# Kernel tuning notes

Measured on AMD Instinct MI355X. Metric: run time of the kernel, lower is better.

The kernel has to match this reference:

```python
import jax, jax.numpy as jnp
import numpy as np

N, E, C, NA, NR, H = 50000, 320000, 64, 10, 8, 64
AVG_NUM_NEIGHBORS = 16.0
WEIGHT_NUMEL = 5 * C  # 5 uvu tensor-product paths, one weight per channel


def setup_inputs() -> dict:
    key = jax.random.key(0)
    ks = jax.random.split(key, 18)
    rn = lambda k, s: jax.random.normal(k, s, dtype=jnp.float32)
    return {
        "node_attrs": jax.random.uniform(ks[0], (N, NA), dtype=jnp.float32),
        "node_feats_s": rn(ks[1], (N, C)),
        "node_feats_v": rn(ks[2], (N, C, 3)),
        "edge_sh0": jnp.ones((E, 1), jnp.float32),          # Y_00 (constant)
        "edge_sh1": rn(ks[3], (E, 3)),                       # Y_1m
        "edge_feats": rn(ks[4], (E, NR)),                    # radial scalars (0e)
        "senders": jax.random.randint(ks[5], (E,), 0, N, dtype=jnp.int32),
        "receivers": jax.random.randint(ks[6], (E,), 0, N, dtype=jnp.int32),
        # skip-connection tensor-product linear: (C*NA)x0e -> Cx0e, (C*NA)x1o -> Cx1o
        "W_sc_s": rn(ks[7], (C * NA, C)),
        "W_sc_v": rn(ks[8], (C * NA, C)),
        # self linear on node_feats (per-irrep channel mixing)
        "W_self_s": rn(ks[9], (C, C)),
        "W_self_v": rn(ks[10], (C, C)),
        # radial MLP: NR -> 64 -> 64 -> 64 -> weight_numel
        "W1": rn(ks[11], (NR, H)),
        "W2": rn(ks[12], (H, H)),
        "W3": rn(ks[13], (H, H)),
        "W4": rn(ks[14], (H, WEIGHT_NUMEL)),
        # output linear: mid irreps 2Cx0e + 3Cx1o -> target Cx0e + Cx1o
        "W_out_s": rn(ks[15], (2 * C, C)),
        "W_out_v": rn(ks[16], (3 * C, C)),
    }


def reference(node_attrs, node_feats_s, node_feats_v, edge_sh0, edge_sh1,
              edge_feats, senders, receivers, W_sc_s, W_sc_v, W_self_s,
              W_self_v, W1, W2, W3, W4, W_out_s, W_out_v):
    n, c = node_feats_s.shape
    na = node_attrs.shape[1]
    # ---- skip connection: Linear(hidden)(node_feats (x) node_attrs) ----
    ts = (node_feats_s[:, :, None] * node_attrs[:, None, :]).reshape(n, c * na)
    tv = (node_feats_v[:, :, None, :] * node_attrs[:, None, :, None]).reshape(n, c * na, 3)
    inv_sc = 1.0 / np.sqrt(c * na)
    sc_s = (ts @ W_sc_s) * inv_sc
    sc_v = jnp.einsum('nkx,kd->ndx', tv, W_sc_v) * inv_sc
    # ---- self linear on node_feats ----
    inv_c = 1.0 / np.sqrt(c)
    s = (node_feats_s @ W_self_s) * inv_c
    v = jnp.einsum('ncx,cd->ndx', node_feats_v, W_self_v) * inv_c
    # ---- radial MLP -> per-edge tensor-product weights ----
    h = jax.nn.silu((edge_feats @ W1) / np.sqrt(edge_feats.shape[1]))
    h = jax.nn.silu((h @ W2) / np.sqrt(H))
    h = jax.nn.silu((h @ W3) / np.sqrt(H))
    w = (h @ W4) / np.sqrt(H)                      # [E, 5C]
    w1, w2, w3, w4, w5 = jnp.split(w, 5, axis=1)   # one weight per path per channel
    # ---- gather -> per-edge equivariant tensor product -> scatter-add ----
    se = s[senders]                                # [E, C]
    ve = v[senders]                                # [E, C, 3]
    p1 = w1 * se * edge_sh0                                              # 0e x 0e -> 0e
    p2 = w2 * jnp.einsum('ecx,ex->ec', ve, edge_sh1) / np.sqrt(3.0)      # 1o x 1o -> 0e
    p3 = (w3 * se)[:, :, None] * edge_sh1[:, None, :]                    # 0e x 1o -> 1o
    p4 = (w4 * edge_sh0)[:, :, None] * ve                                # 1o x 0e -> 1o
    p5 = w5[:, :, None] * jnp.cross(ve, edge_sh1[:, None, :]) / np.sqrt(2.0)  # 1o x 1o -> 1o
    mji_s = jnp.concatenate([p1, p2], axis=1)      # [E, 2C]
    mji_v = jnp.concatenate([p3, p4, p5], axis=1)  # [E, 3C, 3]
    m_s = jnp.zeros((n, 2 * c), mji_s.dtype).at[receivers].add(mji_s)
    m_v = jnp.zeros((n, 3 * c, 3), mji_v.dtype).at[receivers].add(mji_v)
    # ---- output linear / avg_num_neighbors ----
    out_s = (m_s @ W_out_s) / (np.sqrt(2 * c) * AVG_NUM_NEIGHBORS)
    out_v = jnp.einsum('nkx,kd->ndx', m_v, W_out_v) / (np.sqrt(3 * c) * AVG_NUM_NEIGHBORS)
    return (out_s, out_v, sc_s, sc_v)
```

## Files before the change

### kernel.cpp

```cpp
#include <hip/hip_runtime.h>

#define NC    64
#define NATTR 10
#define NH    64
#define NRAD  8
#define TEB   128
#define MPN   704

__device__ __forceinline__ float silu_f(float x) { return x / (1.0f + __expf(-x)); }

typedef __fp16 h2v __attribute__((ext_vector_type(2)));

__device__ __forceinline__ unsigned int pkh(float lo, float hi)
{
    union { h2v h; unsigned int u; } cv;
    cv.h = __builtin_amdgcn_cvt_pkrtz(lo, hi);
    return cv.u;
}
__device__ __forceinline__ h2v uph(unsigned int u)
{
    union { unsigned int u; h2v h; } cv;
    cv.u = u;
    return cv.h;
}

#if defined(__has_builtin)
#if __has_builtin(__builtin_amdgcn_fdot2)
#define HAS_FDOT2 1
#endif
#endif

__device__ __forceinline__ float fd2(unsigned int a, unsigned int b, float c)
{
#ifdef HAS_FDOT2
    return __builtin_amdgcn_fdot2(uph(a), uph(b), c, false);
#else
    h2v x = uph(a), y = uph(b);
    return c + (float)x[0] * (float)y[0] + (float)x[1] * (float)y[1];
#endif
}

__device__ __forceinline__ void dot2w(const uint4* hp,
    const unsigned int (&Wa)[32], const unsigned int (&Wb)[32],
    float& ra, float& rb)
{
    float a = 0.f, b = 0.f;
    #pragma unroll
    for (int q8 = 0; q8 < 8; q8++) {
        uint4 hu = hp[q8];
        unsigned int hw[4] = {hu.x, hu.y, hu.z, hu.w};
        #pragma unroll
        for (int k = 0; k < 4; k++) {
            a = fd2(hw[k], Wa[q8 * 4 + k], a);
            b = fd2(hw[k], Wb[q8 * 4 + k], b);
        }
    }
    ra = a * 0.125f; rb = b * 0.125f;
}

__device__ __forceinline__ void dot3w(const uint4* hp,
    const unsigned int (&Wa)[32], const unsigned int (&Wb)[32],
    const unsigned int (&Wc)[32],
    float& ra, float& rb, float& rc)
{
    float a = 0.f, b = 0.f, c = 0.f;
    #pragma unroll
    for (int q8 = 0; q8 < 8; q8++) {
        uint4 hu = hp[q8];
        unsigned int hw[4] = {hu.x, hu.y, hu.z, hu.w};
        #pragma unroll
        for (int k = 0; k < 4; k++) {
            a = fd2(hw[k], Wa[q8 * 4 + k], a);
            b = fd2(hw[k], Wb[q8 * 4 + k], b);
            c = fd2(hw[k], Wc[q8 * 4 + k], c);
        }
    }
    ra = a * 0.125f; rb = b * 0.125f; rc = c * 0.125f;
}


__global__ void hist_kernel(const int* __restrict__ rcv, int* __restrict__ deg, int E)
{
    int e = blockIdx.x * 256 + threadIdx.x;
    if (e < E) atomicAdd(&deg[rcv[e]], 1);
}

__global__ __launch_bounds__(256)
void scan_kernel(const int* __restrict__ deg, int* __restrict__ row_ptr, int N)
{
    __shared__ int sums[256];
    __shared__ int offs[257];
    const int t = threadIdx.x;
    const int chunk = (N + 255) / 256;
    int b = t * chunk, e = min(N, b + chunk);
    int s = 0;
    for (int k = b; k < e; k++) s += deg[k];
    sums[t] = s;
    __syncthreads();
    if (t == 0) {
        int run = 0;
        for (int i = 0; i < 256; i++) { offs[i] = run; run += sums[i]; }
        offs[256] = run;
    }
    __syncthreads();
    int run = offs[t];
    for (int k = b; k < e; k++) { row_ptr[k] = run; run += deg[k]; }
    if (t == 255) row_ptr[N] = offs[256];
}

__global__ void fill_kernel(const int* __restrict__ rcv, const int* __restrict__ row_ptr,
                            int* __restrict__ cursor, int* __restrict__ eidx, int E)
{
    int e = blockIdx.x * 256 + threadIdx.x;
    if (e < E) {
        int r = rcv[e];
        int pos = atomicAdd(&cursor[r], 1);
        eidx[row_ptr[r] + pos] = e;
    }
}

__global__ __launch_bounds__(256)
void self_kernel(const float* __restrict__ fs, const float* __restrict__ fv,
                 const float* __restrict__ Wes, const float* __restrict__ Wev,
                 float* __restrict__ out, int N)
{
    __shared__ float s_l[4][NC];
    __shared__ float v_l[4][3][NC];
    const int t = threadIdx.x, wv = t >> 6, lane = t & 63;
    const int n = blockIdx.x * 4 + wv;

    if (n < N) {
        s_l[wv][lane] = fs[(size_t)n * NC + lane];
        v_l[wv][0][lane] = fv[(size_t)n * NC * 3 + lane * 3 + 0];
        v_l[wv][1][lane] = fv[(size_t)n * NC * 3 + lane * 3 + 1];
        v_l[wv][2][lane] = fv[(size_t)n * NC * 3 + lane * 3 + 2];
    }
    __syncthreads();
    if (n >= N) return;

    const int d = lane;
    float a = 0.f, bx = 0.f, by = 0.f, bz = 0.f;
    #pragma unroll 8
    for (int c = 0; c < NC; c++) {
        float ws = Wes[c * NC + d];
        float wvv = Wev[c * NC + d];
        a  += s_l[wv][c] * ws;
        bx += v_l[wv][0][c] * wvv;
        by += v_l[wv][1][c] * wvv;
        bz += v_l[wv][2][c] * wvv;
    }
    out[(size_t)N * 256 + (size_t)n * NC + d]            = a  * 0.125f;
    out[(size_t)N * 320 + (size_t)n * 192 +       d]     = bx * 0.125f;
    out[(size_t)N * 320 + (size_t)n * 192 +  64 + d]     = by * 0.125f;
    out[(size_t)N * 320 + (size_t)n * 192 + 128 + d]     = bz * 0.125f;
}

__global__ __launch_bounds__(128, 3)
void edge_kernel(const float* __restrict__ ef, const float* __restrict__ sh0,
                 const float* __restrict__ sh1,
                 const int* __restrict__ snd, const int* __restrict__ rcv,
                 const float* __restrict__ W1, const float* __restrict__ W2,
                 const float* __restrict__ W3, const float* __restrict__ W4,
                 const float* __restrict__ s_st, const float* __restrict__ v_st,
                 const int* __restrict__ eidx,
                 float* __restrict__ m, int E)
{
    __shared__ unsigned int h_l[TEB][36];
    __shared__ float sh1_l[TEB][3];
    __shared__ float sh0_l[TEB];
    __shared__ int   snd_l[TEB];
    __shared__ int   rcv_l[TEB];

    const int t = threadIdx.x;
    const int p0 = blockIdx.x * TEB;

    {
        int p = p0 + t;
        bool valid = p < E;
        int e = valid ? eidx[p] : 0;
        snd_l[t] = valid ? snd[e] : 0;
        rcv_l[t] = valid ? rcv[e] : -1;
        sh0_l[t] = valid ? sh0[e] : 0.f;
        sh1_l[t][0] = valid ? sh1[(size_t)e * 3 + 0] : 0.f;
        sh1_l[t][1] = valid ? sh1[(size_t)e * 3 + 1] : 0.f;
        sh1_l[t][2] = valid ? sh1[(size_t)e * 3 + 2] : 0.f;

        float x[NRAD];
        #pragma unroll
        for (int r = 0; r < NRAD; r++)
            x[r] = valid ? ef[(size_t)e * NRAD + r] : 0.f;

        float h1[NH];
        #pragma unroll
        for (int j = 0; j < NH; j++) {
            float a = 0.f;
            #pragma unroll
            for (int r = 0; r < NRAD; r++) a += x[r] * W1[r * NH + j];
            h1[j] = silu_f(a * 0.35355339059327373f);
        }

        unsigned int h2p[32];
        for (int jt = 0; jt < 16; jt++) {
            float a0 = 0.f, a1 = 0.f, a2 = 0.f, a3 = 0.f;
            #pragma unroll
            for (int c = 0; c < NH; c++) {
                float hv = h1[c];
                const float* wr = W2 + c * NH + jt * 4;
                a0 += hv * wr[0]; a1 += hv * wr[1];
                a2 += hv * wr[2]; a3 += hv * wr[3];
            }
            h2p[jt * 2 + 0] = pkh(silu_f(a0 * 0.125f), silu_f(a1 * 0.125f));
            h2p[jt * 2 + 1] = pkh(silu_f(a2 * 0.125f), silu_f(a3 * 0.125f));
        }
        for (int jt = 0; jt < 16; jt++) {
            float a0 = 0.f, a1 = 0.f, a2 = 0.f, a3 = 0.f;
            #pragma unroll
            for (int cp = 0; cp < 32; cp++) {
                h2v u = uph(h2p[cp]);
                float hl = (float)u[0], hh = (float)u[1];
                const float* wr0 = W3 + (2 * cp) * NH + jt * 4;
                const float* wr1 = W3 + (2 * cp + 1) * NH + jt * 4;
                a0 += hl * wr0[0] + hh * wr1[0];
                a1 += hl * wr0[1] + hh * wr1[1];
                a2 += hl * wr0[2] + hh * wr1[2];
                a3 += hl * wr0[3] + hh * wr1[3];
            }
            h_l[t][jt * 2 + 0] = pkh(silu_f(a0 * 0.125f), silu_f(a1 * 0.125f));
            h_l[t][jt * 2 + 1] = pkh(silu_f(a2 * 0.125f), silu_f(a3 * 0.125f));
        }
    }
    __syncthreads();

    const int wv = t >> 6, lane = t & 63;
    const int base = wv * 64;
    const int v_sd = snd_l[base + lane];
    const int v_rc = rcv_l[base + lane];

    {
        unsigned int WA[32], WC[32];
        #pragma unroll
        for (int q = 0; q < 32; q++) {
            WA[q] = pkh(W4[(2 * q) * 320 + lane],       W4[(2 * q + 1) * 320 + lane]);
            WC[q] = pkh(W4[(2 * q) * 320 + 128 + lane], W4[(2 * q + 1) * 320 + 128 + lane]);
        }
        #pragma unroll
        for (int q = 0; q < 32; q++) {
            asm volatile("" : "+v"(WA[q]));
            asm volatile("" : "+v"(WC[q]));
        }
        float g0 = s_st[(size_t)__builtin_amdgcn_readlane(v_sd, 0) * NC + lane];
        float g1 = s_st[(size_t)__builtin_amdgcn_readlane(v_sd, 1) * NC + lane];
        float g2 = s_st[(size_t)__builtin_amdgcn_readlane(v_sd, 2) * NC + lane];
        float g3 = s_st[(size_t)__builtin_amdgcn_readlane(v_sd, 3) * NC + lane];
        int r_cur = -1;
        float a1 = 0.f, a3x = 0.f, a3y = 0.f, a3z = 0.f;
        #pragma unroll 4
        for (int ei = 0; ei < 64; ei++) {
            const int pn = (ei + 4 > 63) ? 63 : ei + 4;
            const float gf = s_st[(size_t)__builtin_amdgcn_readlane(v_sd, pn) * NC + lane];
            const int r = __builtin_amdgcn_readlane(v_rc, ei);
            if (r != r_cur) {
                if (r_cur >= 0) {
                    float* mb = m + (size_t)r_cur * MPN;
                    unsafeAtomicAdd(mb + lane,             a1);
                    unsafeAtomicAdd(mb + 128 + lane,       a3x);
                    unsafeAtomicAdd(mb + 128 + 192 + lane, a3y);
                    unsafeAtomicAdd(mb + 128 + 384 + lane, a3z);
                    a1 = a3x = a3y = a3z = 0.f;
                }
                r_cur = r;
            }
            if (r >= 0) {
                const int pos = base + ei;
                float w1w, w3w;
                dot2w((const uint4*)(&h_l[pos][0]), WA, WC, w1w, w3w);
                float se = g0;
                a1 += w1w * se * sh0_l[pos];
                float t3 = w3w * se;
                a3x += t3 * sh1_l[pos][0];
                a3y += t3 * sh1_l[pos][1];
                a3z += t3 * sh1_l[pos][2];
            }
            g0 = g1; g1 = g2; g2 = g3; g3 = gf;
        }
        if (r_cur >= 0) {
            float* mb = m + (size_t)r_cur * MPN;
            unsafeAtomicAdd(mb + lane,             a1);
            unsafeAtomicAdd(mb + 128 + lane,       a3x);
            unsafeAtomicAdd(mb + 128 + 192 + lane, a3y);
            unsafeAtomicAdd(mb + 128 + 384 + lane, a3z);
        }
    }

    {
        unsigned int WB[32], WD[32], WE[32];
        #pragma unroll
        for (int q = 0; q < 32; q++) {
            WB[q] = pkh(W4[(2 * q) * 320 +  64 + lane], W4[(2 * q + 1) * 320 +  64 + lane]);
            WD[q] = pkh(W4[(2 * q) * 320 + 192 + lane], W4[(2 * q + 1) * 320 + 192 + lane]);
            WE[q] = pkh(W4[(2 * q) * 320 + 256 + lane], W4[(2 * q + 1) * 320 + 256 + lane]);
        }
        #pragma unroll
        for (int q = 0; q < 32; q++) {
            asm volatile("" : "+v"(WB[q]));
            asm volatile("" : "+v"(WD[q]));
            asm volatile("" : "+v"(WE[q]));
        }
        float gx0, gy0, gz0, gx1, gy1, gz1, gx2, gy2, gz2, gx3, gy3, gz3;
        {
            size_t s0 = (size_t)__builtin_amdgcn_readlane(v_sd, 0) * 192;
            size_t s1 = (size_t)__builtin_amdgcn_readlane(v_sd, 1) * 192;
            size_t s2 = (size_t)__builtin_amdgcn_readlane(v_sd, 2) * 192;
            size_t s3 = (size_t)__builtin_amdgcn_readlane(v_sd, 3) * 192;
            gx0 = v_st[s0 + lane]; gy0 = v_st[s0 + 64 + lane]; gz0 = v_st[s0 + 128 + lane];
            gx1 = v_st[s1 + lane]; gy1 = v_st[s1 + 64 + lane]; gz1 = v_st[s1 + 128 + lane];
            gx2 = v_st[s2 + lane]; gy2 = v_st[s2 + 64 + lane]; gz2 = v_st[s2 + 128 + lane];
            gx3 = v_st[s3 + lane]; gy3 = v_st[s3 + 64 + lane]; gz3 = v_st[s3 + 128 + lane];
        }
        int r_cur = -1;
        float a2 = 0.f;
        float a4x = 0.f, a4y = 0.f, a4z = 0.f;
        float a5x = 0.f, a5y = 0.f, a5z = 0.f;
        #pragma unroll 4
        for (int ei = 0; ei < 64; ei++) {
            const int pn = (ei + 4 > 63) ? 63 : ei + 4;
            size_t sb = (size_t)__builtin_amdgcn_readlane(v_sd, pn) * 192;
            const float gxf = v_st[sb + lane];
            const float gyf = v_st[sb + 64 + lane];
            const float gzf = v_st[sb + 128 + lane];
            const int r = __builtin_amdgcn_readlane(v_rc, ei);
            if (r != r_cur) {
                if (r_cur >= 0) {
                    float* mb = m + (size_t)r_cur * MPN;
                    unsafeAtomicAdd(mb + 64 + lane,              a2);
                    unsafeAtomicAdd(mb + 128 + 64 + lane,        a4x);
                    unsafeAtomicAdd(mb + 128 + 192 + 64 + lane,  a4y);
                    unsafeAtomicAdd(mb + 128 + 384 + 64 + lane,  a4z);
                    unsafeAtomicAdd(mb + 128 + 128 + lane,       a5x);
                    unsafeAtomicAdd(mb + 128 + 192 + 128 + lane, a5y);
                    unsafeAtomicAdd(mb + 128 + 384 + 128 + lane, a5z);
                    a2 = a4x = a4y = a4z = a5x = a5y = a5z = 0.f;
                }
                r_cur = r;
            }
            if (r >= 0) {
                const int pos = base + ei;
                float w2w, w4w, w5w;
                dot3w((const uint4*)(&h_l[pos][0]), WB, WD, WE, w2w, w4w, w5w);
                float vx = gx0, vy = gy0, vz = gz0;
                float shx = sh1_l[pos][0], shy = sh1_l[pos][1], shz = sh1_l[pos][2];
                float dot = vx * shx + vy * shy + vz * shz;
                a2 += w2w * dot * 0.5773502691896258f;
                float w4s = w4w * sh0_l[pos];
                a4x += w4s * vx; a4y += w4s * vy; a4z += w4s * vz;
                float w5s = w5w * 0.7071067811865476f;
                a5x += w5s * (vy * shz - vz * shy);
                a5y += w5s * (vz * shx - vx * shz);
                a5z += w5s * (vx * shy - vy * shx);
            }
            gx0 = gx1; gy0 = gy1; gz0 = gz1;
            gx1 = gx2; gy1 = gy2; gz1 = gz2;
            gx2 = gx3; gy2 = gy3; gz2 = gz3;
            gx3 = gxf; gy3 = gyf; gz3 = gzf;
        }
        if (r_cur >= 0) {
            float* mb = m + (size_t)r_cur * MPN;
            unsafeAtomicAdd(mb + 64 + lane,              a2);
            unsafeAtomicAdd(mb + 128 + 64 + lane,        a4x);
            unsafeAtomicAdd(mb + 128 + 192 + 64 + lane,  a4y);
            unsafeAtomicAdd(mb + 128 + 384 + 64 + lane,  a4z);
            unsafeAtomicAdd(mb + 128 + 128 + lane,       a5x);
            unsafeAtomicAdd(mb + 128 + 192 + 128 + lane, a5y);
            unsafeAtomicAdd(mb + 128 + 384 + 128 + lane, a5z);
        }
    }
}

__global__ __launch_bounds__(256)
void sc_kernel(const float* __restrict__ attrs, const float* __restrict__ fs,
               const float* __restrict__ fv,
               const float* __restrict__ Wss, const float* __restrict__ Wsv,
               float* __restrict__ out, int N)
{
    __shared__ unsigned int At[32][68];
    __shared__ unsigned int Bt[32][68];

    const int part = blockIdx.y;
    const int n0 = blockIdx.x * 64;
    const int t = threadIdx.x;
    const int tn = t & 15, td = t >> 4;
    const float* W = (part == 0) ? Wss : Wsv;
    const int x = part - 1;

    float acc[4][4];
    #pragma unroll
    for (int i = 0; i < 4; i++)
        #pragma unroll
        for (int j = 0; j < 4; j++) acc[i][j] = 0.f;

    for (int kt = 0; kt < 10; kt++) {
        __syncthreads();
        for (int i = t; i < 2048; i += 256) {
            int n = i >> 5, kp = i & 31;
            int k0 = kt * 64 + kp * 2;
            int c0 = k0 / 10, a0 = k0 - c0 * 10;
            int k1 = k0 + 1;
            int c1 = k1 / 10, a1 = k1 - c1 * 10;
            int ng = n0 + n;
            float f0 = 0.f, f1 = 0.f;
            if (ng < N) {
                float fa = (part == 0) ? fs[(size_t)ng * 64 + c0]
                                       : fv[((size_t)ng * 64 + c0) * 3 + x];
                float fb = (part == 0) ? fs[(size_t)ng * 64 + c1]
                                       : fv[((size_t)ng * 64 + c1) * 3 + x];
                f0 = fa * attrs[(size_t)ng * 10 + a0];
                f1 = fb * attrs[(size_t)ng * 10 + a1];
            }
            At[kp][n] = pkh(f0, f1);
        }
        for (int i = t; i < 2048; i += 256) {
            int kp = i >> 6, d = i & 63;
            Bt[kp][d] = pkh(W[(size_t)(kt * 64 + 2 * kp) * 64 + d],
                            W[(size_t)(kt * 64 + 2 * kp + 1) * 64 + d]);
        }
        __syncthreads();
        #pragma unroll 8
        for (int kp = 0; kp < 32; kp++) {
            uint4 au = *(const uint4*)(&At[kp][tn * 4]);
            uint4 bu = *(const uint4*)(&Bt[kp][td * 4]);
            unsigned int aa[4] = {au.x, au.y, au.z, au.w};
            unsigned int bb[4] = {bu.x, bu.y, bu.z, bu.w};
            #pragma unroll
            for (int i = 0; i < 4; i++)
                #pragma unroll
                for (int j = 0; j < 4; j++)
                    acc[i][j] = fd2(aa[i], bb[j], acc[i][j]);
        }
    }

    const float inv_sc = 0.03952847075210474f;
    #pragma unroll
    for (int i = 0; i < 4; i++) {
        int ng = n0 + tn * 4 + i;
        if (ng >= N) continue;
        #pragma unroll
        for (int j = 0; j < 4; j++) {
            int d = td * 4 + j;
            float v = acc[i][j] * inv_sc;
            if (part == 0) out[(size_t)N * 256 + (size_t)ng * 64 + d] = v;
            else           out[(size_t)N * 320 + (size_t)ng * 192 + d * 3 + x] = v;
        }
    }
}

__global__ __launch_bounds__(256)
void outlin_kernel(const float* __restrict__ m,
                   const float* __restrict__ Wos, const float* __restrict__ Wov,
                   float* __restrict__ out, int N)
{
    __shared__ unsigned int At[32][68];
    __shared__ unsigned int Bt[32][68];

    const int part = blockIdx.y;
    const int n0 = blockIdx.x * 64;
    const int t = threadIdx.x;
    const int tn = t & 15, td = t >> 4;
    const int x = part - 1;
    const int ntiles = (part == 0) ? 2 : 3;
    const int aoff = (part == 0) ? 0 : 128 + x * 192;
    const float* W = (part == 0) ? Wos : Wov;

    float acc[4][4];
    #pragma unroll
    for (int i = 0; i < 4; i++)
        #pragma unroll
        for (int j = 0; j < 4; j++) acc[i][j] = 0.f;

    for (int kt = 0; kt < ntiles; kt++) {
        __syncthreads();
        for (int i = t; i < 2048; i += 256) {
            int n = i >> 5, kp = i & 31;
            int ng = n0 + n;
            float f0 = 0.f, f1 = 0.f;
            if (ng < N) {
                const float* mp = m + (size_t)ng * MPN + aoff + kt * 64 + kp * 2;
                f0 = mp[0]; f1 = mp[1];
            }
            At[kp][n] = pkh(f0, f1);
        }
        for (int i = t; i < 2048; i += 256) {
            int kp = i >> 6, d = i & 63;
            Bt[kp][d] = pkh(W[(size_t)(kt * 64 + 2 * kp) * 64 + d],
                            W[(size_t)(kt * 64 + 2 * kp + 1) * 64 + d]);
        }
        __syncthreads();
        #pragma unroll 8
        for (int kp = 0; kp < 32; kp++) {
            uint4 au = *(const uint4*)(&At[kp][tn * 4]);
            uint4 bu = *(const uint4*)(&Bt[kp][td * 4]);
            unsigned int aa[4] = {au.x, au.y, au.z, au.w};
            unsigned int bb[4] = {bu.x, bu.y, bu.z, bu.w};
            #pragma unroll
            for (int i = 0; i < 4; i++)
                #pragma unroll
                for (int j = 0; j < 4; j++)
                    acc[i][j] = fd2(aa[i], bb[j], acc[i][j]);
        }
    }

    const float scale = (part == 0) ? 0.005524271728019903f
                                    : 0.004510527174164819f;
    #pragma unroll
    for (int i = 0; i < 4; i++) {
        int ng = n0 + tn * 4 + i;
        if (ng >= N) continue;
        #pragma unroll
        for (int j = 0; j < 4; j++) {
            int d = td * 4 + j;
            float v = acc[i][j] * scale;
            if (part == 0) out[(size_t)ng * 64 + d] = v;
            else           out[(size_t)N * 64 + (size_t)ng * 192 + d * 3 + x] = v;
        }
    }
}

extern "C" void kernel_launch(void* const* d_in, const int* in_sizes, int n_in,
                              void* d_out, int out_size, void* d_ws, size_t ws_size,
                              hipStream_t stream)
{
    const float* attrs = (const float*)d_in[0];
    const float* fs    = (const float*)d_in[1];
    const float* fv    = (const float*)d_in[2];
    const float* sh0   = (const float*)d_in[3];
    const float* sh1   = (const float*)d_in[4];
    const float* ef    = (const float*)d_in[5];
    const int*   snd   = (const int*)d_in[6];
    const int*   rcv   = (const int*)d_in[7];
    const float* Wss   = (const float*)d_in[8];
    const float* Wsv   = (const float*)d_in[9];
    const float* Wes   = (const float*)d_in[10];
    const float* Wev   = (const float*)d_in[11];
    const float* W1    = (const float*)d_in[12];
    const float* W2    = (const float*)d_in[13];
    const float* W3    = (const float*)d_in[14];
    const float* W4    = (const float*)d_in[15];
    const float* Wos   = (const float*)d_in[16];
    const float* Wov   = (const float*)d_in[17];

    const int N = in_sizes[0] / NATTR;
    const int E = in_sizes[6];

    float* out = (float*)d_out;
    const float* s_st = out + (size_t)N * 256;
    const float* v_st = out + (size_t)N * 320;

    int* deg     = (int*)d_out;
    int* cursor  = deg + N;
    int* row_ptr = cursor + N;
    int* eidx    = row_ptr + N + 1;

    float* m = (float*)d_ws;

    (void)hipMemsetAsync(deg, 0, (size_t)2 * N * sizeof(int), stream);
    (void)hipMemsetAsync(m, 0, (size_t)N * MPN * sizeof(float), stream);

    const int eb = (E + 255) / 256;
    hist_kernel<<<eb, 256, 0, stream>>>(rcv, deg, E);
    scan_kernel<<<1, 256, 0, stream>>>(deg, row_ptr, N);
    fill_kernel<<<eb, 256, 0, stream>>>(rcv, row_ptr, cursor, eidx, E);

    self_kernel<<<(N + 3) / 4, 256, 0, stream>>>(fs, fv, Wes, Wev, out, N);

    const int nbe = (E + TEB - 1) / TEB;
    edge_kernel<<<nbe, 128, 0, stream>>>(ef, sh0, sh1, snd, rcv,
                                         W1, W2, W3, W4, s_st, v_st,
                                         eidx, m, E);

    dim3 g_out((N + 63) / 64, 4);
    outlin_kernel<<<g_out, 256, 0, stream>>>(m, Wos, Wov, out, N);

    dim3 g_sc((N + 63) / 64, 4);
    sc_kernel<<<g_sc, 256, 0, stream>>>(attrs, fs, fv, Wss, Wsv, out, N);
}
```

Before: 1.073 ms.

## Merge skip-connection and output-linear GEMMs into one kernel with larger node tiles

Replaces the separate sc_kernel and outlin_kernel with one post_kernel. It launches on a grid of 8 parts and uses 256-node tiles with a 16x4 register accumulator per thread, so each loaded weight tile is reused across four times as many nodes. The edge kernel also packs sh0 and sh1 into one float4 shared array so a single vector LDS load replaces four scalar loads. Costs are higher register pressure and more LDS per block, which lowers occupancy, plus fewer and larger blocks that can cause load imbalance between the sc and outlin parts.

```diff
diff --git a/kernel.cpp b/kernel.cpp
--- a/kernel.cpp
+++ b/kernel.cpp
@@ -166,8 +166,7 @@
                  float* __restrict__ m, int E)
 {
     __shared__ unsigned int h_l[TEB][36];
-    __shared__ float sh1_l[TEB][3];
-    __shared__ float sh0_l[TEB];
+    __shared__ float sh_l[TEB][4];
     __shared__ int   snd_l[TEB];
     __shared__ int   rcv_l[TEB];
 
@@ -180,10 +179,10 @@
         int e = valid ? eidx[p] : 0;
         snd_l[t] = valid ? snd[e] : 0;
         rcv_l[t] = valid ? rcv[e] : -1;
-        sh0_l[t] = valid ? sh0[e] : 0.f;
-        sh1_l[t][0] = valid ? sh1[(size_t)e * 3 + 0] : 0.f;
-        sh1_l[t][1] = valid ? sh1[(size_t)e * 3 + 1] : 0.f;
-        sh1_l[t][2] = valid ? sh1[(size_t)e * 3 + 2] : 0.f;
+        sh_l[t][0] = valid ? sh0[e] : 0.f;
+        sh_l[t][1] = valid ? sh1[(size_t)e * 3 + 0] : 0.f;
+        sh_l[t][2] = valid ? sh1[(size_t)e * 3 + 1] : 0.f;
+        sh_l[t][3] = valid ? sh1[(size_t)e * 3 + 2] : 0.f;
 
         float x[NRAD];
         #pragma unroll
@@ -274,12 +273,13 @@
                 const int pos = base + ei;
                 float w1w, w3w;
                 dot2w((const uint4*)(&h_l[pos][0]), WA, WC, w1w, w3w);
+                float4 sh4 = *(const float4*)(&sh_l[pos][0]);
                 float se = g0;
-                a1 += w1w * se * sh0_l[pos];
+                a1 += w1w * se * sh4.x;
                 float t3 = w3w * se;
-                a3x += t3 * sh1_l[pos][0];
-                a3y += t3 * sh1_l[pos][1];
-                a3z += t3 * sh1_l[pos][2];
+                a3x += t3 * sh4.y;
+                a3y += t3 * sh4.z;
+                a3z += t3 * sh4.w;
             }
             g0 = g1; g1 = g2; g2 = g3; g3 = gf;
         }
@@ -347,16 +347,16 @@
                 const int pos = base + ei;
                 float w2w, w4w, w5w;
                 dot3w((const uint4*)(&h_l[pos][0]), WB, WD, WE, w2w, w4w, w5w);
+                float4 sh4 = *(const float4*)(&sh_l[pos][0]);
                 float vx = gx0, vy = gy0, vz = gz0;
-                float shx = sh1_l[pos][0], shy = sh1_l[pos][1], shz = sh1_l[pos][2];
-                float dot = vx * shx + vy * shy + vz * shz;
+                float dot = vx * sh4.y + vy * sh4.z + vz * sh4.w;
                 a2 += w2w * dot * 0.5773502691896258f;
-                float w4s = w4w * sh0_l[pos];
+                float w4s = w4w * sh4.x;
                 a4x += w4s * vx; a4y += w4s * vy; a4z += w4s * vz;
                 float w5s = w5w * 0.7071067811865476f;
-                a5x += w5s * (vy * shz - vz * shy);
-                a5y += w5s * (vz * shx - vx * shz);
-                a5z += w5s * (vx * shy - vy * shx);
+                a5x += w5s * (vy * sh4.w - vz * sh4.z);
+                a5y += w5s * (vz * sh4.y - vx * sh4.w);
+                a5z += w5s * (vx * sh4.z - vy * sh4.y);
             }
             gx0 = gx1; gy0 = gy1; gz0 = gz1;
             gx1 = gx2; gy1 = gy2; gz1 = gz2;
@@ -377,46 +377,71 @@
 }
 
 __global__ __launch_bounds__(256)
-void sc_kernel(const float* __restrict__ attrs, const float* __restrict__ fs,
-               const float* __restrict__ fv,
-               const float* __restrict__ Wss, const float* __restrict__ Wsv,
-               float* __restrict__ out, int N)
-{
-    __shared__ unsigned int At[32][68];
+void post_kernel(const float* __restrict__ attrs, const float* __restrict__ fs,
+                 const float* __restrict__ fv,
+                 const float* __restrict__ Wss, const float* __restrict__ Wsv,
+                 const float* __restrict__ m,
+                 const float* __restrict__ Wos, const float* __restrict__ Wov,
+                 float* __restrict__ out, int N)
+{
+    __shared__ unsigned int At[32][260];
     __shared__ unsigned int Bt[32][68];
 
-    const int part = blockIdx.y;
-    const int n0 = blockIdx.x * 64;
+    const int y = blockIdx.y;
+    const bool is_sc = (y < 4);
+    const int part = is_sc ? y : y - 4;
+    const int n0 = blockIdx.x * 256;
     const int t = threadIdx.x;
     const int tn = t & 15, td = t >> 4;
-    const float* W = (part == 0) ? Wss : Wsv;
     const int x = part - 1;
 
-    float acc[4][4];
+    const float* W;
+    int nkt, aoff = 0;
+    if (is_sc) { W = (part == 0) ? Wss : Wsv; nkt = 10; }
+    else {
+        W = (part == 0) ? Wos : Wov;
+        nkt = (part == 0) ? 2 : 3;
+        aoff = (part == 0) ? 0 : 128 + x * 192;
+    }
+
+    float acc[16][4];
     #pragma unroll
-    for (int i = 0; i < 4; i++)
+    for (int i = 0; i < 16; i++)
         #pragma unroll
         for (int j = 0; j < 4; j++) acc[i][j] = 0.f;
 
-    for (int kt = 0; kt < 10; kt++) {
+    for (int kt = 0; kt < nkt; kt++) {
         __syncthreads();
-        for (int i = t; i < 2048; i += 256) {
-            int n = i >> 5, kp = i & 31;
-            int k0 = kt * 64 + kp * 2;
-            int c0 = k0 / 10, a0 = k0 - c0 * 10;
-            int k1 = k0 + 1;
-            int c1 = k1 / 10, a1 = k1 - c1 * 10;
-            int ng = n0 + n;
-            float f0 = 0.f, f1 = 0.f;
-            if (ng < N) {
-                float fa = (part == 0) ? fs[(size_t)ng * 64 + c0]
-                                       : fv[((size_t)ng * 64 + c0) * 3 + x];
-                float fb = (part == 0) ? fs[(size_t)ng * 64 + c1]
-                                       : fv[((size_t)ng * 64 + c1) * 3 + x];
-                f0 = fa * attrs[(size_t)ng * 10 + a0];
-                f1 = fb * attrs[(size_t)ng * 10 + a1];
-            }
-            At[kp][n] = pkh(f0, f1);
+        if (is_sc) {
+            for (int i = t; i < 8192; i += 256) {
+                int n = i >> 5, kp = i & 31;
+                int k0 = kt * 64 + kp * 2;
+                int c0 = k0 / 10, am0 = k0 - c0 * 10;
+                int k1 = k0 + 1;
+                int c1 = k1 / 10, am1 = k1 - c1 * 10;
+                int ng = n0 + n;
+                float f0 = 0.f, f1 = 0.f;
+                if (ng < N) {
+                    float fa = (part == 0) ? fs[(size_t)ng * 64 + c0]
+                                           : fv[((size_t)ng * 64 + c0) * 3 + x];
+                    float fb = (part == 0) ? fs[(size_t)ng * 64 + c1]
+                                           : fv[((size_t)ng * 64 + c1) * 3 + x];
+                    f0 = fa * attrs[(size_t)ng * 10 + am0];
+                    f1 = fb * attrs[(size_t)ng * 10 + am1];
+                }
+                At[kp][n] = pkh(f0, f1);
+            }
+        } else {
+            for (int i = t; i < 8192; i += 256) {
+                int n = i >> 5, kp = i & 31;
+                int ng = n0 + n;
+                float f0 = 0.f, f1 = 0.f;
+                if (ng < N) {
+                    const float* mp = m + (size_t)ng * MPN + aoff + kt * 64 + kp * 2;
+                    f0 = mp[0]; f1 = mp[1];
+                }
+                At[kp][n] = pkh(f0, f1);
+            }
         }
         for (int i = t; i < 2048; i += 256) {
             int kp = i >> 6, d = i & 63;
@@ -424,102 +449,46 @@
                             W[(size_t)(kt * 64 + 2 * kp + 1) * 64 + d]);
         }
         __syncthreads();
-        #pragma unroll 8
+        #pragma unroll 4
         for (int kp = 0; kp < 32; kp++) {
-            uint4 au = *(const uint4*)(&At[kp][tn * 4]);
             uint4 bu = *(const uint4*)(&Bt[kp][td * 4]);
-            unsigned int aa[4] = {au.x, au.y, au.z, au.w};
             unsigned int bb[4] = {bu.x, bu.y, bu.z, bu.w};
             #pragma unroll
-            for (int i = 0; i < 4; i++)
+            for (int sb = 0; sb < 4; sb++) {
+                uint4 au = *(const uint4*)(&At[kp][sb * 64 + tn * 4]);
+                unsigned int aa[4] = {au.x, au.y, au.z, au.w};
                 #pragma unroll
-                for (int j = 0; j < 4; j++)
-                    acc[i][j] = fd2(aa[i], bb[j], acc[i][j]);
-        }
-    }
-
-    const float inv_sc = 0.03952847075210474f;
+                for (int i = 0; i < 4; i++)
+                    #pragma unroll
+                    for (int j = 0; j < 4; j++)
+                        acc[sb * 4 + i][j] = fd2(aa[i], bb[j], acc[sb * 4 + i][j]);
+            }
+        }
+    }
+
+    float scale;
+    if (is_sc) scale = 0.03952847075210474f;
+    else scale = (part == 0) ? 0.005524271728019903f
+                             : 0.004510527174164819f;
+
     #pragma unroll
-    for (int i = 0; i < 4; i++) {
-        int ng = n0 + tn * 4 + i;
-        if (ng >= N) continue;
-        #pragma unroll
-        for (int j = 0; j < 4; j++) {
-            int d = td * 4 + j;
-            float v = acc[i][j] * inv_sc;
-            if (part == 0) out[(size_t)N * 256 + (size_t)ng * 64 + d] = v;
-            else           out[(size_t)N * 320 + (size_t)ng * 192 + d * 3 + x] = v;
-        }
-    }
-}
-
-__global__ __launch_bounds__(256)
-void outlin_kernel(const float* __restrict__ m,
-                   const float* __restrict__ Wos, const float* __restrict__ Wov,
-                   float* __restrict__ out, int N)
-{
-    __shared__ unsigned int At[32][68];
-    __shared__ unsigned int Bt[32][68];
-
-    const int part = blockIdx.y;
-    const int n0 = blockIdx.x * 64;
-    const int t = threadIdx.x;
-    const int tn = t & 15, td = t >> 4;
-    const int x = part - 1;
-    const int ntiles = (part == 0) ? 2 : 3;
-    const int aoff = (part == 0) ? 0 : 128 + x * 192;
-    const float* W = (part == 0) ? Wos : Wov;
-
-    float acc[4][4];
-    #pragma unroll
-    for (int i = 0; i < 4; i++)
-        #pragma unroll
-        for (int j = 0; j < 4; j++) acc[i][j] = 0.f;
-
-    for (int kt = 0; kt < ntiles; kt++) {
-        __syncthreads();
-        for (int i = t; i < 2048; i += 256) {
-            int n = i >> 5, kp = i & 31;
-            int ng = n0 + n;
-            float f0 = 0.f, f1 = 0.f;
-            if (ng < N) {
-                const float* mp = m + (size_t)ng * MPN + aoff + kt * 64 + kp * 2;
-                f0 = mp[0]; f1 = mp[1];
-            }
-            At[kp][n] = pkh(f0, f1);
-        }
-        for (int i = t; i < 2048; i += 256) {
-            int kp = i >> 6, d = i & 63;
-            Bt[kp][d] = pkh(W[(size_t)(kt * 64 + 2 * kp) * 64 + d],
-                            W[(size_t)(kt * 64 + 2 * kp + 1) * 64 + d]);
-        }
-        __syncthreads();
-        #pragma unroll 8
-        for (int kp = 0; kp < 32; kp++) {
-            uint4 au = *(const uint4*)(&At[kp][tn * 4]);
-            uint4 bu = *(const uint4*)(&Bt[kp][td * 4]);
-            unsigned int aa[4] = {au.x, au.y, au.z, au.w};
-            unsigned int bb[4] = {bu.x, bu.y, bu.z, bu.w};
+    for (int sb = 0; sb < 4; sb++) {
+        #pragma unroll
+        for (int i = 0; i < 4; i++) {
+            int ng = n0 + sb * 64 + tn * 4 + i;
+            if (ng >= N) continue;
             #pragma unroll
-            for (int i = 0; i < 4; i++)
-                #pragma unroll
-                for (int j = 0; j < 4; j++)
-                    acc[i][j] = fd2(aa[i], bb[j], acc[i][j]);
-        }
-    }
-
-    const float scale = (part == 0) ? 0.005524271728019903f
-                                    : 0.004510527174164819f;
-    #pragma unroll
-    for (int i = 0; i < 4; i++) {
-        int ng = n0 + tn * 4 + i;
-        if (ng >= N) continue;
-        #pragma unroll
-        for (int j = 0; j < 4; j++) {
-            int d = td * 4 + j;
-            float v = acc[i][j] * scale;
-            if (part == 0) out[(size_t)ng * 64 + d] = v;
-            else           out[(size_t)N * 64 + (size_t)ng * 192 + d * 3 + x] = v;
+            for (int j = 0; j < 4; j++) {
+                int d = td * 4 + j;
+                float v = acc[sb * 4 + i][j] * scale;
+                if (is_sc) {
+                    if (part == 0) out[(size_t)N * 256 + (size_t)ng * 64 + d] = v;
+                    else           out[(size_t)N * 320 + (size_t)ng * 192 + d * 3 + x] = v;
+                } else {
+                    if (part == 0) out[(size_t)ng * 64 + d] = v;
+                    else           out[(size_t)N * 64 + (size_t)ng * 192 + d * 3 + x] = v;
+                }
+            }
         }
     }
 }
@@ -576,9 +545,7 @@
                                          W1, W2, W3, W4, s_st, v_st,
                                          eidx, m, E);
 
-    dim3 g_out((N + 63) / 64, 4);
-    outlin_kernel<<<g_out, 256, 0, stream>>>(m, Wos, Wov, out, N);
-
-    dim3 g_sc((N + 63) / 64, 4);
-    sc_kernel<<<g_sc, 256, 0, stream>>>(attrs, fs, fv, Wss, Wsv, out, N);
-}
+    dim3 g_post((N + 255) / 256, 8);
+    post_kernel<<<g_post, 256, 0, stream>>>(attrs, fs, fv, Wss, Wsv,
+                                            m, Wos, Wov, out, N);
+}
```

Measured after the change: 1.194 ms. 1.11x slower.
